# Optimization experiments

Measured on AMD Instinct MI355X. Metric: run time of the kernel, lower is better.

Reference implementation:

```python
import jax, jax.numpy as jnp
import numpy as np

LEVELS = (1, 2, 4)
NHEAD = 4
LN_EPS = 1e-5


def _layernorm(x, g, b):
    m = jnp.mean(x, axis=-1, keepdims=True)
    v = jnp.mean((x - m) ** 2, axis=-1, keepdims=True)
    return (x - m) * jax.lax.rsqrt(v + LN_EPS) * g + b


def _spp_pool(x, starts, ends):
    # Exact AdaptiveAvgPool1d over per-proposal segments via inclusive-prefix-sum.
    # x: [B,C,T]; starts/ends: [B,P] int. Returns [B, P, C*sum(LEVELS)].
    B, C, T = x.shape
    P = starts.shape[1]
    xt = jnp.transpose(x, (0, 2, 1))  # [B,T,C]
    csum = jnp.concatenate([jnp.zeros((B, 1, C), x.dtype), jnp.cumsum(xt, axis=1)], axis=1)  # [B,T+1,C]
    n = ends - starts  # [B,P], always >= 1
    feats = []
    for L in LEVELS:
        i = jnp.arange(L)
        lo = (starts[..., None] + (i * n[..., None]) // L).reshape(B, P * L)
        hi = (starts[..., None] + ((i + 1) * n[..., None] + L - 1) // L).reshape(B, P * L)
        slo = jnp.take_along_axis(csum, lo[..., None], axis=1)  # [B,P*L,C]
        shi = jnp.take_along_axis(csum, hi[..., None], axis=1)
        mean = (shi - slo) / (hi - lo).astype(x.dtype)[..., None]
        # torch view(N, C*L) flattens [C,L] C-major -> transpose bins to last axis
        feats.append(mean.reshape(B, P, L, C).transpose(0, 1, 3, 2).reshape(B, P, C * L))
    return jnp.concatenate(feats, axis=-1)


def _encoder_layer(x, qkv_w, qkv_b, out_w, out_b, g1, b1, w1, bb1, w2, bb2, g2, b2):
    # Post-norm nn.TransformerEncoderLayer with exact-erf gelu, dropout=0 (eval)
    B, P, d = x.shape
    dh = d // NHEAD
    qkv = x @ qkv_w.T + qkv_b  # [B,P,3d]
    q, k, v = jnp.split(qkv, 3, axis=-1)
    sh = lambda t: t.reshape(B, P, NHEAD, dh).transpose(0, 2, 1, 3)  # [B,H,P,dh]
    q, k, v = sh(q), sh(k), sh(v)
    scale = 1.0 / float(np.sqrt(dh))
    attn = jax.nn.softmax(jnp.einsum('bhqd,bhkd->bhqk', q, k) * scale, axis=-1)
    o = jnp.einsum('bhqk,bhkd->bhqd', attn, v).transpose(0, 2, 1, 3).reshape(B, P, d)
    o = o @ out_w.T + out_b
    x = _layernorm(x + o, g1, b1)
    h = jax.nn.gelu(x @ w1.T + bb1, approximate=False) @ w2.T + bb2
    return _layernorm(x + h, g2, b2)


def _forward(x, proposal_boxes, proj_w, proj_b, pos_w1, pos_b1, pos_w2, pos_b2,
             qkv_w, qkv_b, out_w, out_b, ln1_g, ln1_b, ff1_w, ff1_b,
             ff2_w, ff2_b, ln2_g, ln2_b, cls_w, cls_b, det_w, det_b):
    B, C, T = x.shape
    P = proposal_boxes.shape[1]
    starts = jnp.clip(proposal_boxes[..., 0], 0, T - 1)
    ends = jnp.clip(proposal_boxes[..., 1], 1, T)
    ends = jnp.where(ends <= starts, jnp.minimum(starts + 1, T), ends)
    feats = _spp_pool(x, starts, ends)  # [B,P,spp_out_dim]
    s_f = proposal_boxes[..., 0].astype(x.dtype)
    e_f = proposal_boxes[..., 1].astype(x.dtype)
    centers = (s_f + e_f) / 2.0
    lengths = jnp.maximum(e_f - s_f, 1.0)
    pos_feat = jnp.stack([centers / T, lengths / T], axis=-1)  # [B,P,2]
    sort_idx = jnp.argsort(centers, axis=1)
    feats_s = jnp.take_along_axis(feats, sort_idx[..., None], axis=1)
    pos_emb = jax.nn.relu(pos_feat @ pos_w1.T + pos_b1) @ pos_w2.T + pos_b2
    pos_emb_s = jnp.take_along_axis(pos_emb, sort_idx[..., None], axis=1)
    tok = feats_s @ proj_w.T + proj_b + pos_emb_s  # [B,P,d]
    for l in range(qkv_w.shape[0]):
        tok = _encoder_layer(tok, qkv_w[l], qkv_b[l], out_w[l], out_b[l],
                             ln1_g[l], ln1_b[l], ff1_w[l], ff1_b[l],
                             ff2_w[l], ff2_b[l], ln2_g[l], ln2_b[l])
    inv = jnp.argsort(sort_idx, axis=1)
    ctx = jnp.take_along_axis(tok, inv[..., None], axis=1)  # [B,P,d]
    class_logits = ctx @ cls_w.T + cls_b  # [B,P,nc]
    det_logits = ctx @ det_w.T + det_b
    class_prob = jax.nn.softmax(class_logits, axis=2)
    det_prob = jax.nn.softmax(det_logits, axis=1)
    joint_prob = class_prob * det_prob
    video_prob = joint_prob.sum(axis=1)
    return video_prob, joint_prob, class_logits, det_logits, ctx


def setup_inputs() -> dict:
    key = jax.random.key(0)
    ks = jax.random.split(key, 32)
    B, C, T, P = 8, 512, 2048, 512
    d, dff, nc, nl = 512, 1024, 30, 2
    spp_out = C * sum(LEVELS)
    s = 0.02
    f32 = jnp.float32
    inp = {
        'x': jax.random.normal(ks[0], (B, C, T), f32),
        'proposal_boxes': jax.random.randint(ks[1], (B, P, 2), 0, T).astype(jnp.int32),
        'proj_w': jax.random.normal(ks[2], (d, spp_out), f32) * s,
        'proj_b': jnp.zeros((d,), f32),
        'pos_w1': jax.random.normal(ks[3], (d, 2), f32) * s,
        'pos_b1': jnp.zeros((d,), f32),
        'pos_w2': jax.random.normal(ks[4], (d, d), f32) * s,
        'pos_b2': jnp.zeros((d,), f32),
        'qkv_w': jax.random.normal(ks[5], (nl, 3 * d, d), f32) * s,
        'qkv_b': jnp.zeros((nl, 3 * d), f32),
        'out_w': jax.random.normal(ks[6], (nl, d, d), f32) * s,
        'out_b': jnp.zeros((nl, d), f32),
        'ln1_g': jnp.ones((nl, d), f32),
        'ln1_b': jnp.zeros((nl, d), f32),
        'ff1_w': jax.random.normal(ks[7], (nl, dff, d), f32) * s,
        'ff1_b': jnp.zeros((nl, dff), f32),
        'ff2_w': jax.random.normal(ks[8], (nl, d, dff), f32) * s,
        'ff2_b': jnp.zeros((nl, d), f32),
        'ln2_g': jnp.ones((nl, d), f32),
        'ln2_b': jnp.zeros((nl, d), f32),
        'cls_w': jax.random.normal(ks[9], (nc, d), f32) * s,
        'cls_b': jnp.zeros((nc,), f32),
        'det_w': jax.random.normal(ks[10], (nc, d), f32) * s,
        'det_b': jnp.zeros((nc,), f32),
    }
    return inp


def reference(x, proposal_boxes, proj_w, proj_b, pos_w1, pos_b1, pos_w2, pos_b2,
              qkv_w, qkv_b, out_w, out_b, ln1_g, ln1_b, ff1_w, ff1_b,
              ff2_w, ff2_b, ln2_g, ln2_b, cls_w, cls_b, det_w, det_b):
    return _forward(x, proposal_boxes, proj_w, proj_b, pos_w1, pos_b1, pos_w2, pos_b2,
                    qkv_w, qkv_b, out_w, out_b, ln1_g, ln1_b, ff1_w, ff1_b,
                    ff2_w, ff2_b, ln2_g, ln2_b, cls_w, cls_b, det_w, det_b)
```

## Files before the change

kernel.cpp:

```cpp
#include <hip/hip_runtime.h>

#define TDIM 2048
#define CDIM 512
#define BDIM 8
#define PDIM 512
#define DMODEL 512
#define NCOUT 30
#define SPPOUT 3584
#define AKDIM 4096

typedef __attribute__((ext_vector_type(8))) short short8;
typedef __attribute__((ext_vector_type(4))) short short4v;
typedef __attribute__((ext_vector_type(4))) float f32x4;

typedef const __attribute__((address_space(1))) void* as1cv;
typedef __attribute__((address_space(3))) void* as3v;

__device__ __forceinline__ void gl_lds16(const short* g, short* l){
  __builtin_amdgcn_global_load_lds((as1cv)g, (as3v)l, 16, 0, 0);
}

__device__ __forceinline__ short f2b(float f){
  unsigned u = __float_as_uint(f);
  unsigned r = (u + 0x7fffu + ((u >> 16) & 1u)) >> 16;
  return (short)r;
}

__device__ __forceinline__ float waveSum(float v){
#pragma unroll
  for (int o = 32; o > 0; o >>= 1) v += __shfl_xor(v, o);
  return v;
}
__device__ __forceinline__ float waveMax(float v){
#pragma unroll
  for (int o = 32; o > 0; o >>= 1) v = fmaxf(v, __shfl_xor(v, o));
  return v;
}

__global__ void kprep2(const float* __restrict__ pw, const float* __restrict__ pw2,
                       const float* __restrict__ qw, const float* __restrict__ ow,
                       const float* __restrict__ f1, const float* __restrict__ f2,
                       const float* __restrict__ cl, const float* __restrict__ dt,
                       const float* __restrict__ pb, const float* __restrict__ pb2,
                       const float* __restrict__ cb, const float* __restrict__ db,
                       short* __restrict__ Wc, short* __restrict__ Wd,
                       float* __restrict__ bc, float* __restrict__ bh){
  int i = blockIdx.x * 256 + threadIdx.x;
  if (i < 2097152){
    int r = i >> 12, k = i & 4095;
    float v = (k < SPPOUT) ? pw[(size_t)r * SPPOUT + k] : pw2[(size_t)r * DMODEL + (k - SPPOUT)];
    Wc[i] = f2b(v);
  } else if (i < 6322176){
    int j = i - 2097152;
    float v;
    if (j < 1572864) v = qw[j];
    else if (j < 2097152) v = ow[j - 1572864];
    else if (j < 3145728) v = f1[j - 2097152];
    else if (j < 4194304) v = f2[j - 3145728];
    else if (j < 4209664) v = cl[j - 4194304];
    else v = dt[j - 4209664];
    Wd[j] = f2b(v);
  } else {
    int k = i - 6322176;
    if (k < 512) bc[k] = pb[k] + pb2[k];
    else if (k < 572) bh[k - 512] = (k < 542) ? cb[k - 512] : db[k - 542];
  }
}

__global__ void kscan(const float* __restrict__ x, float* __restrict__ W, float* __restrict__ tot){
  int idx = blockIdx.x;
  int b = idx >> 5, rem = idx & 31, ch = rem >> 1, cg = rem & 1;
  int c = cg * 256 + threadIdx.x;
  const float* xp = x + ((size_t)(b * CDIM + c)) * TDIM + ch * 128;
  float* wp = W + ((size_t)b * TDIM + ch * 128) * CDIM + c;
  float run = 0.f;
  for (int tl = 0; tl < 128; tl += 4){
    float4 v = *(const float4*)(xp + tl);
    run += v.x; wp[(size_t)(tl + 0) * CDIM] = run;
    run += v.y; wp[(size_t)(tl + 1) * CDIM] = run;
    run += v.z; wp[(size_t)(tl + 2) * CDIM] = run;
    run += v.w; wp[(size_t)(tl + 3) * CDIM] = run;
  }
  tot[((size_t)b * 16 + ch) * CDIM + c] = run;
}

__global__ void koff(const float* __restrict__ tot, float* __restrict__ off){
  int b = blockIdx.x >> 1, cg = blockIdx.x & 1;
  int c = cg * 256 + threadIdx.x;
  float run = 0.f;
  for (int ch = 0; ch < 16; ++ch){
    off[((size_t)b * 16 + ch) * CDIM + c] = run;
    run += tot[((size_t)b * 16 + ch) * CDIM + c];
  }
}

__global__ void ksort(const int* __restrict__ boxes, int* __restrict__ sidx, float* __restrict__ out){
  __shared__ unsigned key[PDIM];
  int b = blockIdx.x, t = threadIdx.x;
  if (b == 0 && t < 240) out[t] = 0.f;
  int s = boxes[(size_t)(b * PDIM + t) * 2];
  int e = boxes[(size_t)(b * PDIM + t) * 2 + 1];
  key[t] = ((unsigned)(s + e) << 9) | (unsigned)t;
  __syncthreads();
  for (int k = 2; k <= PDIM; k <<= 1){
    for (int j = k >> 1; j > 0; j >>= 1){
      int ixj = t ^ j;
      if (ixj > t){
        unsigned a = key[t], c2 = key[ixj];
        bool up = ((t & k) == 0);
        bool doswap = up ? (a > c2) : (a < c2);
        if (doswap){ key[t] = c2; key[ixj] = a; }
      }
      __syncthreads();
    }
  }
  sidx[b * PDIM + t] = (int)(key[t] & 511u);
}

__global__ void kspp(const float* __restrict__ W, const float* __restrict__ off,
                     const int* __restrict__ boxes, const int* __restrict__ sidx,
                     const float* __restrict__ pw1, const float* __restrict__ pb1,
                     short* __restrict__ A){
  int blk = blockIdx.x;
  int b = blk >> 9, j = blk & 511;
  int p = sidx[b * PDIM + j];
  int s0 = boxes[(size_t)(b * PDIM + p) * 2];
  int e0 = boxes[(size_t)(b * PDIM + p) * 2 + 1];
  int start = min(max(s0, 0), TDIM - 1);
  int end   = min(max(e0, 1), TDIM);
  if (end <= start) end = min(start + 1, TDIM);
  int n = end - start;

  int lo[7], hi[7], cb[7], cl[7];
  {
    const int Ls[3] = {1, 2, 4};
    const int Bo[3] = {0, 512, 1536};
    int q = 0;
    for (int li = 0; li < 3; ++li){
      int L = Ls[li];
      for (int i = 0; i < L; ++i){
        lo[q] = start + (i * n) / L;
        hi[q] = start + ((i + 1) * n + L - 1) / L;
        cb[q] = Bo[li] + i;
        cl[q] = L;
        ++q;
      }
    }
  }
  float s_f = (float)s0, e_f = (float)e0;
  float px = (s_f + e_f) * 0.5f / (float)TDIM;
  float py = fmaxf(e_f - s_f, 1.f) / (float)TDIM;
  short* Ar = A + (size_t)(b * PDIM + j) * AKDIM;
  const float* Wb = W + (size_t)b * TDIM * CDIM;
  const float* ob = off + (size_t)b * 16 * CDIM;
  for (int c = threadIdx.x; c < CDIM; c += 256){
#pragma unroll
    for (int q = 0; q < 7; ++q){
      int l = lo[q], h = hi[q];
      float fl = (l == 0) ? 0.f : (Wb[(size_t)(l - 1) * CDIM + c] + ob[((l - 1) >> 7) * CDIM + c]);
      float fh = Wb[(size_t)(h - 1) * CDIM + c] + ob[((h - 1) >> 7) * CDIM + c];
      Ar[cb[q] + c * cl[q]] = f2b((fh - fl) / (float)(h - l));
    }
    float hv = pw1[c * 2] * px + pw1[c * 2 + 1] * py + pb1[c];
    Ar[SPPOUT + c] = f2b(fmaxf(hv, 0.f));
  }
}

template<int BN, int SWZ = 0>
__global__ __launch_bounds__(256) void gemm_bt(
    int M, int N, int K,
    const short* __restrict__ A, int lda, long long sAb, long long sAh,
    const short* __restrict__ B, int ldb, long long sBb, long long sBh,
    float* __restrict__ Cf, short* __restrict__ Cb, int ldc, long long sCb, long long sCh,
    int hdiv, float alpha,
    const float* __restrict__ bias, const float* __restrict__ resid, int act,
    short* __restrict__ Vtp)
{
  constexpr int JF = BN / 32;
  __shared__ short smem[128 * 64 + BN * 64];
  short* As = smem;
  short* Bs = smem + 128 * 64;
  int bx = blockIdx.x, by = blockIdx.y, bz = blockIdx.z;
  if constexpr (SWZ){
    int nx = gridDim.x, ny = gridDim.y;
    int rt = ny >> 3;
    int flat = (bz * ny + by) * nx + bx;
    int xcd = flat & 7, wl = flat >> 3;
    by = xcd * rt + wl % rt;
    int rest = wl / rt;
    bx = rest % nx;
    bz = rest / nx;
  }
  int zb = bz / hdiv, zh = bz - zb * hdiv;
  A += (size_t)zb * sAb + (size_t)zh * sAh;
  B += (size_t)zb * sBb + (size_t)zh * sBh;
  size_t coff = (size_t)zb * sCb + (size_t)zh * sCh;
  int rowBase = by * 128, colBase = bx * BN;
  int t = threadIdx.x;
  int lane = t & 63;
  int wave = t >> 6;
  int wm = (wave >> 1) * 64, wn = (wave & 1) * (BN / 2);
  int lm = lane & 15, quad = lane >> 4;
  int srow = t >> 3;
  int skw = ((t & 7) * 8) ^ ((srow & 7) * 8);

  const short* Agp[4];
#pragma unroll
  for (int it = 0; it < 4; ++it)
    Agp[it] = A + (size_t)min(rowBase + srow + it * 32, M - 1) * lda + skw;
  const short* Bgp[JF];
#pragma unroll
  for (int it = 0; it < JF; ++it)
    Bgp[it] = B + (size_t)min(colBase + srow + it * 32, N - 1) * ldb + skw;

  f32x4 zero4 = {0.f, 0.f, 0.f, 0.f};
  f32x4 acc[4][JF];
#pragma unroll
  for (int i = 0; i < 4; ++i)
#pragma unroll
    for (int j = 0; j < JF; ++j) acc[i][j] = zero4;

  int axr = (lm & 7) * 8;
  for (int k0 = 0; k0 < K; k0 += 64){
#pragma unroll
    for (int it = 0; it < 4; ++it) gl_lds16(Agp[it] + k0, As + it * 2048 + t * 8);
#pragma unroll
    for (int it = 0; it < JF; ++it) gl_lds16(Bgp[it] + k0, Bs + it * 2048 + t * 8);
    __syncthreads();
#pragma unroll
    for (int h = 0; h < 2; ++h){
      int koff = (h * 32 + quad * 8) ^ axr;
      short8 af[4], bfr[JF];
#pragma unroll
      for (int i = 0; i < 4; ++i)
        af[i] = *(const short8*)(As + (wm + i * 16 + lm) * 64 + koff);
#pragma unroll
      for (int j = 0; j < JF; ++j)
        bfr[j] = *(const short8*)(Bs + (wn + j * 16 + lm) * 64 + koff);
#pragma unroll
      for (int i = 0; i < 4; ++i)
#pragma unroll
        for (int j = 0; j < JF; ++j)
          acc[i][j] = __builtin_amdgcn_mfma_f32_16x16x32_bf16(af[i], bfr[j], acc[i][j], 0, 0, 0);
    }
    __syncthreads();
  }

  if (Vtp && colBase >= 1024){
    short* LT = smem;
#pragma unroll
    for (int i = 0; i < 4; ++i){
#pragma unroll
      for (int j = 0; j < JF; ++j){
        int d = wn + j * 16 + lm;
        int prow = wm + i * 16 + quad * 4;
        short4v pk;
#pragma unroll
        for (int r = 0; r < 4; ++r){
          float v = acc[i][j][r] * alpha;
          if (bias) v += bias[colBase + d];
          pk[r] = f2b(v);
        }
        *(short4v*)(LT + d * 132 + prow) = pk;
      }
    }
    __syncthreads();
    int bb = rowBase >> 9;
    int hh = (colBase - 1024) >> 7;
    int dd0 = (colBase - 1024) & 127;
    int dl = t >> 2, pl = (t & 3) * 32;
    const short* sp = LT + dl * 132 + pl;
    short* dp = Vtp + ((size_t)(bb * 4 + hh)) * 65536 + (size_t)(dd0 + dl) * 512 + (rowBase & 511) + pl;
#pragma unroll
    for (int u = 0; u < 4; ++u) *(short8*)(dp + u * 8) = *(const short8*)(sp + u * 8);
    return;
  }

#pragma unroll
  for (int i = 0; i < 4; ++i){
#pragma unroll
    for (int j = 0; j < JF; ++j){
#pragma unroll
      for (int r = 0; r < 4; ++r){
        int row = rowBase + wm + i * 16 + quad * 4 + r;
        int col = colBase + wn + j * 16 + lm;
        if (row < M && col < N){
          float v = acc[i][j][r] * alpha;
          if (bias) v += bias[col];
          size_t ci = coff + (size_t)row * ldc + col;
          if (resid) v += resid[ci];
          if (act) v = 0.5f * v * (1.f + erff(v * 0.7071067811865476f));
          if (Cf) Cf[ci] = v;
          if (Cb) Cb[ci] = f2b(v);
        }
      }
    }
  }
}

__global__ void kredG1(const float* __restrict__ part, const float* __restrict__ bias,
                       float* __restrict__ tok, short* __restrict__ tokb){
  int i = blockIdx.x * 256 + threadIdx.x;
  float v = part[i] + part[i + 2097152] + part[i + 4194304] + part[i + 6291456] + bias[i & 511];
  tok[i] = v;
  tokb[i] = f2b(v);
}

__global__ __launch_bounds__(256) void kflash(const short* __restrict__ qkvb,
                                              const short* __restrict__ Vt,
                                              short* __restrict__ ob){
  __shared__ float Ofs[4][16][128];
  __shared__ float Ml[4][16], Ll[4][16], Fw[4][16], Linv[16];
  int bid = blockIdx.x;
  int bh = bid & 31, qt = bid >> 5;
  int b = bh >> 2, h = bh & 3;
  int t = threadIdx.x;
  int w = t >> 6, lane = t & 63;
  int lm = lane & 15, quad = lane >> 4;
  const float SL2 = 0.1275174468f;

  const short* qbase = qkvb + (size_t)(b * 512 + qt * 16 + lm) * 1536 + h * 128 + quad * 8;
  short8 qf[4];
#pragma unroll
  for (int s = 0; s < 4; ++s) qf[s] = *(const short8*)(qbase + s * 32);

  const short* kbase = qkvb + (size_t)(b * 512) * 1536 + 512 + h * 128 + quad * 8;
  const short* vbase = Vt + (size_t)bh * 65536 + (size_t)lm * 512 + quad * 8;

  f32x4 zero4 = {0.f, 0.f, 0.f, 0.f};
  f32x4 Of[8];
#pragma unroll
  for (int i = 0; i < 8; ++i) Of[i] = zero4;
  float mrun[4] = {-1e30f, -1e30f, -1e30f, -1e30f};
  float lrun[4] = {0.f, 0.f, 0.f, 0.f};
  short* Pw = (short*)&Ofs[w][0][0];

#pragma unroll
  for (int kt = 0; kt < 2; ++kt){
    int kb = w * 128 + kt * 64;
    f32x4 Sf[4];
#pragma unroll
    for (int j = 0; j < 4; ++j) Sf[j] = zero4;
#pragma unroll
    for (int s = 0; s < 4; ++s){
#pragma unroll
      for (int j = 0; j < 4; ++j){
        short8 kf = *(const short8*)(kbase + (size_t)(kb + j * 16 + lm) * 1536 + s * 32);
        Sf[j] = __builtin_amdgcn_mfma_f32_16x16x32_bf16(qf[s], kf, Sf[j], 0, 0, 0);
      }
    }
    float alpha[4];
#pragma unroll
    for (int r = 0; r < 4; ++r){
      float mx = fmaxf(fmaxf(Sf[0][r], Sf[1][r]), fmaxf(Sf[2][r], Sf[3][r])) * SL2;
#pragma unroll
      for (int o = 1; o < 16; o <<= 1) mx = fmaxf(mx, __shfl_xor(mx, o));
      float mnew = fmaxf(mrun[r], mx);
      alpha[r] = exp2f(mrun[r] - mnew);
      float psum = 0.f;
#pragma unroll
      for (int j = 0; j < 4; ++j){
        float p = exp2f(Sf[j][r] * SL2 - mnew);
        Sf[j][r] = p;
        psum += p;
      }
#pragma unroll
      for (int o = 1; o < 16; o <<= 1) psum += __shfl_xor(psum, o);
      lrun[r] = lrun[r] * alpha[r] + psum;
      mrun[r] = mnew;
    }
#pragma unroll
    for (int i = 0; i < 8; ++i)
#pragma unroll
      for (int r = 0; r < 4; ++r) Of[i][r] *= alpha[r];
#pragma unroll
    for (int j = 0; j < 4; ++j)
#pragma unroll
      for (int r = 0; r < 4; ++r){
        int q = quad * 4 + r;
        int key = j * 16 + lm;
        Pw[q * 64 + (key ^ ((q & 7) * 8))] = f2b(Sf[j][r]);
      }
#pragma unroll
    for (int ts = 0; ts < 2; ++ts){
      short8 pa = *(const short8*)(Pw + lm * 64 + (((ts * 32 + quad * 8) ^ ((lm & 7) * 8))));
#pragma unroll
      for (int jd = 0; jd < 8; ++jd){
        short8 vf = *(const short8*)(vbase + (size_t)(jd * 16) * 512 + kb + ts * 32);
        Of[jd] = __builtin_amdgcn_mfma_f32_16x16x32_bf16(pa, vf, Of[jd], 0, 0, 0);
      }
    }
  }

#pragma unroll
  for (int jd = 0; jd < 8; ++jd)
#pragma unroll
    for (int r = 0; r < 4; ++r)
      Ofs[w][quad * 4 + r][jd * 16 + lm] = Of[jd][r];
  if (lm == 0){
#pragma unroll
    for (int r = 0; r < 4; ++r){
      Ml[w][quad * 4 + r] = mrun[r];
      Ll[w][quad * 4 + r] = lrun[r];
    }
  }
  __syncthreads();

  if (t < 64){
    int wv = t >> 4, row = t & 15;
    float M = fmaxf(fmaxf(Ml[0][row], Ml[1][row]), fmaxf(Ml[2][row], Ml[3][row]));
    Fw[wv][row] = exp2f(Ml[wv][row] - M);
    if (wv == 0){
      float lsum = Ll[0][row] * exp2f(Ml[0][row] - M) + Ll[1][row] * exp2f(Ml[1][row] - M)
                 + Ll[2][row] * exp2f(Ml[2][row] - M) + Ll[3][row] * exp2f(Ml[3][row] - M);
      Linv[row] = 1.f / lsum;
    }
  }
  __syncthreads();

  {
    int row = t >> 4, dbase = (t & 15) * 8;
    float f0 = Fw[0][row], f1 = Fw[1][row], f2v = Fw[2][row], f3 = Fw[3][row];
    float li = Linv[row];
    short* dst = ob + ((size_t)(b * 512 + qt * 16 + row)) * 512 + h * 128 + dbase;
#pragma unroll
    for (int u = 0; u < 8; ++u){
      float v = Ofs[0][row][dbase + u] * f0 + Ofs[1][row][dbase + u] * f1
              + Ofs[2][row][dbase + u] * f2v + Ofs[3][row][dbase + u] * f3;
      dst[u] = f2b(v * li);
    }
  }
}

__global__ void klnR(const float* __restrict__ part, const float* __restrict__ bias,
                     const float* __restrict__ resid,
                     const float* __restrict__ g, const float* __restrict__ bb,
                     float* __restrict__ Yf, short* __restrict__ Yb){
  int row = blockIdx.x, lane = threadIdx.x;
  size_t base = (size_t)row * DMODEL;
  float v[8]; float s = 0.f;
#pragma unroll
  for (int i = 0; i < 8; ++i){
    int c = lane + 64 * i;
    v[i] = part[base + c] + part[base + c + 2097152] + part[base + c + 4194304]
         + part[base + c + 6291456] + bias[c] + resid[base + c];
    s += v[i];
  }
  s = waveSum(s);
  float m = s * (1.f / DMODEL);
  float q = 0.f;
#pragma unroll
  for (int i = 0; i < 8; ++i){ float d = v[i] - m; q += d * d; }
  q = waveSum(q);
  float inv = rsqrtf(q * (1.f / DMODEL) + 1e-5f);
#pragma unroll
  for (int i = 0; i < 8; ++i){
    int c = lane + 64 * i;
    float o = (v[i] - m) * inv * g[c] + bb[c];
    Yf[base + c] = o;
    Yb[base + c] = f2b(o);
  }
}

__global__ void kdetsm(const float* __restrict__ hd, float* __restrict__ dp){
  int b = blockIdx.x / NCOUT, c = blockIdx.x % NCOUT, lane = threadIdx.x;
  float v[8]; float m = -1e30f;
#pragma unroll
  for (int i = 0; i < 8; ++i){
    v[i] = hd[((size_t)(b * PDIM) + lane + 64 * i) * 60 + 30 + c];
    m = fmaxf(m, v[i]);
  }
  m = waveMax(m);
  float s = 0.f;
#pragma unroll
  for (int i = 0; i < 8; ++i){ v[i] = expf(v[i] - m); s += v[i]; }
  s = waveSum(s);
  float r = 1.f / s;
#pragma unroll
  for (int i = 0; i < 8; ++i)
    dp[((size_t)(b * PDIM) + lane + 64 * i) * NCOUT + c] = v[i] * r;
}

__global__ void kfinal(const float* __restrict__ hd, const float* __restrict__ dps,
                       const float* __restrict__ tok, const int* __restrict__ sidx,
                       float* __restrict__ out){
  int blk = blockIdx.x;
  int b = blk >> 9, j = blk & 511;
  int lane = threadIdx.x;
  int p = sidx[b * PDIM + j];
  float* video = out;
  float* joint = out + 240;
  float* clso  = out + 123120;
  float* deto  = out + 246000;
  float* ctxo  = out + 368880;
  size_t rs60 = (size_t)(b * PDIM + j) * 60;
  size_t rs30 = (size_t)(b * PDIM + j) * NCOUT;
  size_t ro = (size_t)(b * PDIM + p) * NCOUT;
  float lc = (lane < NCOUT) ? hd[rs60 + lane] : -1e30f;
  float m = waveMax(lc);
  float e = (lane < NCOUT) ? expf(lc - m) : 0.f;
  float s = waveSum(e);
  float cp = e / s;
  if (lane < NCOUT){
    float dv  = hd[rs60 + 30 + lane];
    float dpv = dps[rs30 + lane];
    float jp  = cp * dpv;
    clso[ro + lane] = lc;
    deto[ro + lane] = dv;
    joint[ro + lane] = jp;
    atomicAdd(&video[b * NCOUT + lane], jp);
  }
  const float* tr = tok + (size_t)(b * PDIM + j) * DMODEL;
  float* cr = ctxo + (size_t)(b * PDIM + p) * DMODEL;
  for (int c = lane; c < DMODEL; c += 64) cr[c] = tr[c];
}

extern "C" void kernel_launch(void* const* d_in, const int* in_sizes, int n_in,
                              void* d_out, int out_size, void* d_ws, size_t ws_size,
                              hipStream_t stream) {
  const float* x      = (const float*)d_in[0];
  const int*   boxes  = (const int*)d_in[1];
  const float* proj_w = (const float*)d_in[2];
  const float* proj_b = (const float*)d_in[3];
  const float* pos_w1 = (const float*)d_in[4];
  const float* pos_b1 = (const float*)d_in[5];
  const float* pos_w2 = (const float*)d_in[6];
  const float* pos_b2 = (const float*)d_in[7];
  const float* qkv_w  = (const float*)d_in[8];
  const float* qkv_b  = (const float*)d_in[9];
  const float* out_w  = (const float*)d_in[10];
  const float* out_b  = (const float*)d_in[11];
  const float* ln1_g  = (const float*)d_in[12];
  const float* ln1_b  = (const float*)d_in[13];
  const float* ff1_w  = (const float*)d_in[14];
  const float* ff1_b  = (const float*)d_in[15];
  const float* ff2_w  = (const float*)d_in[16];
  const float* ff2_b  = (const float*)d_in[17];
  const float* ln2_g  = (const float*)d_in[18];
  const float* ln2_b  = (const float*)d_in[19];
  const float* cls_w  = (const float*)d_in[20];
  const float* cls_b  = (const float*)d_in[21];
  const float* det_w  = (const float*)d_in[22];
  const float* det_b  = (const float*)d_in[23];
  float* out = (float*)d_out;
  float* ws  = (float*)d_ws;

  const size_t oR1    = 0;
  const size_t oS     = 9437184;
  const size_t oTok   = 22020096;
  const size_t oTokb  = 24117248;
  const size_t oTok2  = 25165824;
  const size_t oTok2b = 27262976;
  const size_t oWcat  = 28311552;
  const size_t oBcat  = 29360128;
  const size_t oWq    = 29360640;
  const size_t oWo    = 30147072;
  const size_t oWf1   = 30409216;
  const size_t oWf2   = 30933504;
  const size_t oWcls  = 31457792;
  const size_t oTot   = 31473152;
  const size_t oOff   = 31538688;
  const size_t oSidx  = 31604224;
  const size_t oBhead = oTot;

  short* Abf   = (short*)(ws + oR1);
  short* qkvb  = (short*)(ws + oR1);
  short* Vt    = (short*)(ws + oR1 + 3145728);
  short* obufb = (short*)(ws + oR1 + 4194304);
  short* hbufb = (short*)(ws + oR1 + 5242880);
  float* headS = ws + oR1 + 7340032;
  float* dpS   = ws + oR1 + 7585792;
  float* csum  = ws + oS;
  float* Cpart = ws + oS;
  float* Cp2   = ws + oS;
  float* tok   = ws + oTok;
  short* tokb  = (short*)(ws + oTokb);
  float* tok2  = ws + oTok2;
  short* tok2b = (short*)(ws + oTok2b);
  short* Wcatb = (short*)(ws + oWcat);
  float* bcat  = ws + oBcat;
  short* Wq    = (short*)(ws + oWq);
  short* Wo    = (short*)(ws + oWo);
  short* Wf1   = (short*)(ws + oWf1);
  short* Wf2   = (short*)(ws + oWf2);
  short* Whead = (short*)(ws + oWcls);
  float* tot   = ws + oTot;
  float* offp  = ws + oOff;
  int*   sidx  = (int*)(ws + oSidx);
  float* bhead = ws + oBhead;

  kscan<<<256, 256, 0, stream>>>(x, csum, tot);
  koff<<<16, 256, 0, stream>>>(tot, offp);
  ksort<<<BDIM, 512, 0, stream>>>(boxes, sidx, out);
  kprep2<<<24699, 256, 0, stream>>>(proj_w, pos_w2, qkv_w, out_w, ff1_w, ff2_w, cls_w, det_w,
                                    proj_b, pos_b2, cls_b, det_b, Wcatb, Wq, bcat, bhead);
  kspp<<<BDIM * PDIM, 256, 0, stream>>>(csum, offp, boxes, sidx, pos_w1, pos_b1, Abf);

  gemm_bt<64, 1><<<dim3(8, 32, 4), 256, 0, stream>>>(
      4096, 512, 1024, Abf, 4096, 1024, 0, Wcatb, 4096, 1024, 0,
      Cpart, nullptr, 512, 2097152, 0, 1, 1.f, nullptr, nullptr, 0, nullptr);
  kredG1<<<8192, 256, 0, stream>>>(Cpart, bcat, tok, tokb);

  for (int l = 0; l < 2; ++l){
    const short* qw  = Wq  + (size_t)l * 1536 * 512;
    const short* ow  = Wo  + (size_t)l * 512 * 512;
    const short* f1w = Wf1 + (size_t)l * 1024 * 512;
    const short* f2w = Wf2 + (size_t)l * 512 * 1024;
    const float* qb  = qkv_b + (size_t)l * 1536;
    const float* obv = out_b + (size_t)l * 512;
    const float* f1b = ff1_b + (size_t)l * 1024;
    const float* f2b_ = ff2_b + (size_t)l * 512;

    gemm_bt<64><<<dim3(24, 32, 1), 256, 0, stream>>>(
        4096, 1536, 512, tokb, 512, 0, 0, qw, 512, 0, 0,
        nullptr, qkvb, 1536, 0, 0, 1, 1.f, qb, nullptr, 0, Vt);
    kflash<<<1024, 256, 0, stream>>>(qkvb, Vt, obufb);
    gemm_bt<64><<<dim3(8, 32, 4), 256, 0, stream>>>(
        4096, 512, 128, obufb, 512, 128, 0, ow, 512, 128, 0,
        Cp2, nullptr, 512, 2097152, 0, 1, 1.f, nullptr, nullptr, 0, nullptr);
    klnR<<<4096, 64, 0, stream>>>(Cp2, obv, tok, ln1_g + l * 512, ln1_b + l * 512, tok2, tok2b);
    gemm_bt<64><<<dim3(16, 32, 1), 256, 0, stream>>>(
        4096, 1024, 512, tok2b, 512, 0, 0, f1w, 512, 0, 0,
        nullptr, hbufb, 1024, 0, 0, 1, 1.f, f1b, nullptr, 1, nullptr);
    gemm_bt<64><<<dim3(8, 32, 4), 256, 0, stream>>>(
        4096, 512, 256, hbufb, 1024, 256, 0, f2w, 1024, 256, 0,
        Cp2, nullptr, 512, 2097152, 0, 1, 1.f, nullptr, nullptr, 0, nullptr);
    klnR<<<4096, 64, 0, stream>>>(Cp2, f2b_, tok2, ln2_g + l * 512, ln2_b + l * 512, tok, tokb);
  }

  gemm_bt<64><<<dim3(1, 32, 1), 256, 0, stream>>>(
      4096, 60, 512, tokb, 512, 0, 0, Whead, 512, 0, 0,
      headS, nullptr, 60, 0, 0, 1, 1.f, bhead, nullptr, 0, nullptr);
  kdetsm<<<BDIM * NCOUT, 64, 0, stream>>>(headS, dpS);
  kfinal<<<BDIM * PDIM, 64, 0, stream>>>(headS, dpS, tok, sidx, out);
}
```

Measured before the change: 522.6 us.

## Fuse prep kernels, move offsets into kspp, halve split-K, vectorize reductions

```diff
diff --git a/kernel.cpp b/kernel.cpp
--- a/kernel.cpp
+++ b/kernel.cpp
@@ -37,92 +37,97 @@
   return v;
 }
 
-__global__ void kprep2(const float* __restrict__ pw, const float* __restrict__ pw2,
-                       const float* __restrict__ qw, const float* __restrict__ ow,
-                       const float* __restrict__ f1, const float* __restrict__ f2,
-                       const float* __restrict__ cl, const float* __restrict__ dt,
-                       const float* __restrict__ pb, const float* __restrict__ pb2,
-                       const float* __restrict__ cb, const float* __restrict__ db,
-                       short* __restrict__ Wc, short* __restrict__ Wd,
-                       float* __restrict__ bc, float* __restrict__ bh){
-  int i = blockIdx.x * 256 + threadIdx.x;
-  if (i < 2097152){
-    int r = i >> 12, k = i & 4095;
-    float v = (k < SPPOUT) ? pw[(size_t)r * SPPOUT + k] : pw2[(size_t)r * DMODEL + (k - SPPOUT)];
-    Wc[i] = f2b(v);
-  } else if (i < 6322176){
-    int j = i - 2097152;
-    float v;
-    if (j < 1572864) v = qw[j];
-    else if (j < 2097152) v = ow[j - 1572864];
-    else if (j < 3145728) v = f1[j - 2097152];
-    else if (j < 4194304) v = f2[j - 3145728];
-    else if (j < 4209664) v = cl[j - 4194304];
-    else v = dt[j - 4209664];
-    Wd[j] = f2b(v);
+__global__ __launch_bounds__(512) void k0(
+    const float* __restrict__ x, const int* __restrict__ boxes,
+    const float* __restrict__ pw, const float* __restrict__ pw2,
+    const float* __restrict__ qw, const float* __restrict__ ow,
+    const float* __restrict__ f1, const float* __restrict__ f2,
+    const float* __restrict__ cl, const float* __restrict__ dt,
+    const float* __restrict__ pb, const float* __restrict__ pb2,
+    const float* __restrict__ cb, const float* __restrict__ db,
+    float* __restrict__ W, float* __restrict__ tot,
+    int* __restrict__ sidx, float* __restrict__ out,
+    short* __restrict__ Wc, short* __restrict__ Wd,
+    float* __restrict__ bc, float* __restrict__ bh)
+{
+  __shared__ unsigned key[PDIM];
+  int blk = blockIdx.x, t = threadIdx.x;
+  if (blk < 128){
+    int b = blk >> 4, ch = blk & 15;
+    int c = t;
+    const float* xp = x + ((size_t)(b * CDIM + c)) * TDIM + ch * 128;
+    float* wp = W + ((size_t)b * TDIM + ch * 128) * CDIM + c;
+    float run = 0.f;
+    for (int tl = 0; tl < 128; tl += 4){
+      float4 v = *(const float4*)(xp + tl);
+      run += v.x; wp[(size_t)(tl + 0) * CDIM] = run;
+      run += v.y; wp[(size_t)(tl + 1) * CDIM] = run;
+      run += v.z; wp[(size_t)(tl + 2) * CDIM] = run;
+      run += v.w; wp[(size_t)(tl + 3) * CDIM] = run;
+    }
+    tot[((size_t)b * 16 + ch) * CDIM + c] = run;
+  } else if (blk < 136){
+    int b = blk - 128;
+    if (b == 0 && t < 240) out[t] = 0.f;
+    int s = boxes[(size_t)(b * PDIM + t) * 2];
+    int e = boxes[(size_t)(b * PDIM + t) * 2 + 1];
+    key[t] = ((unsigned)(s + e) << 9) | (unsigned)t;
+    __syncthreads();
+    for (int k = 2; k <= PDIM; k <<= 1){
+      for (int j = k >> 1; j > 0; j >>= 1){
+        int ixj = t ^ j;
+        if (ixj > t){
+          unsigned a = key[t], c2 = key[ixj];
+          bool up = ((t & k) == 0);
+          bool doswap = up ? (a > c2) : (a < c2);
+          if (doswap){ key[t] = c2; key[ixj] = a; }
+        }
+        __syncthreads();
+      }
+    }
+    sidx[b * PDIM + t] = (int)(key[t] & 511u);
   } else {
-    int k = i - 6322176;
-    if (k < 512) bc[k] = pb[k] + pb2[k];
-    else if (k < 572) bh[k - 512] = (k < 542) ? cb[k - 512] : db[k - 542];
-  }
-}
-
-__global__ void kscan(const float* __restrict__ x, float* __restrict__ W, float* __restrict__ tot){
-  int idx = blockIdx.x;
-  int b = idx >> 5, rem = idx & 31, ch = rem >> 1, cg = rem & 1;
-  int c = cg * 256 + threadIdx.x;
-  const float* xp = x + ((size_t)(b * CDIM + c)) * TDIM + ch * 128;
-  float* wp = W + ((size_t)b * TDIM + ch * 128) * CDIM + c;
-  float run = 0.f;
-  for (int tl = 0; tl < 128; tl += 4){
-    float4 v = *(const float4*)(xp + tl);
-    run += v.x; wp[(size_t)(tl + 0) * CDIM] = run;
-    run += v.y; wp[(size_t)(tl + 1) * CDIM] = run;
-    run += v.z; wp[(size_t)(tl + 2) * CDIM] = run;
-    run += v.w; wp[(size_t)(tl + 3) * CDIM] = run;
-  }
-  tot[((size_t)b * 16 + ch) * CDIM + c] = run;
-}
-
-__global__ void koff(const float* __restrict__ tot, float* __restrict__ off){
-  int b = blockIdx.x >> 1, cg = blockIdx.x & 1;
-  int c = cg * 256 + threadIdx.x;
-  float run = 0.f;
-  for (int ch = 0; ch < 16; ++ch){
-    off[((size_t)b * 16 + ch) * CDIM + c] = run;
-    run += tot[((size_t)b * 16 + ch) * CDIM + c];
-  }
-}
-
-__global__ void ksort(const int* __restrict__ boxes, int* __restrict__ sidx, float* __restrict__ out){
-  __shared__ unsigned key[PDIM];
-  int b = blockIdx.x, t = threadIdx.x;
-  if (b == 0 && t < 240) out[t] = 0.f;
-  int s = boxes[(size_t)(b * PDIM + t) * 2];
-  int e = boxes[(size_t)(b * PDIM + t) * 2 + 1];
-  key[t] = ((unsigned)(s + e) << 9) | (unsigned)t;
-  __syncthreads();
-  for (int k = 2; k <= PDIM; k <<= 1){
-    for (int j = k >> 1; j > 0; j >>= 1){
-      int ixj = t ^ j;
-      if (ixj > t){
-        unsigned a = key[t], c2 = key[ixj];
-        bool up = ((t & k) == 0);
-        bool doswap = up ? (a > c2) : (a < c2);
-        if (doswap){ key[t] = c2; key[ixj] = a; }
-      }
-      __syncthreads();
-    }
-  }
-  sidx[b * PDIM + t] = (int)(key[t] & 511u);
-}
-
-__global__ void kspp(const float* __restrict__ W, const float* __restrict__ off,
+    int i = (blk - 136) * 512 + t;
+    if (i < 2097152){
+      int r = i >> 12, k = i & 4095;
+      float v = (k < SPPOUT) ? pw[(size_t)r * SPPOUT + k] : pw2[(size_t)r * DMODEL + (k - SPPOUT)];
+      Wc[i] = f2b(v);
+    } else if (i < 6322176){
+      int j = i - 2097152;
+      float v;
+      if (j < 1572864) v = qw[j];
+      else if (j < 2097152) v = ow[j - 1572864];
+      else if (j < 3145728) v = f1[j - 2097152];
+      else if (j < 4194304) v = f2[j - 3145728];
+      else if (j < 4209664) v = cl[j - 4194304];
+      else v = dt[j - 4209664];
+      Wd[j] = f2b(v);
+    } else {
+      int k = i - 6322176;
+      if (k < 512) bc[k] = pb[k] + pb2[k];
+      else if (k < 572) bh[k - 512] = (k < 542) ? cb[k - 512] : db[k - 542];
+    }
+  }
+}
+
+__global__ void kspp(const float* __restrict__ W, const float* __restrict__ tot,
                      const int* __restrict__ boxes, const int* __restrict__ sidx,
                      const float* __restrict__ pw1, const float* __restrict__ pb1,
                      short* __restrict__ A){
+  __shared__ float offs[16][CDIM];
   int blk = blockIdx.x;
   int b = blk >> 9, j = blk & 511;
+#pragma unroll
+  for (int half = 0; half < 2; ++half){
+    int cc = threadIdx.x + half * 256;
+    float run = 0.f;
+#pragma unroll
+    for (int ch = 0; ch < 16; ++ch){
+      offs[ch][cc] = run;
+      run += tot[((size_t)b * 16 + ch) * CDIM + cc];
+    }
+  }
+  __syncthreads();
   int p = sidx[b * PDIM + j];
   int s0 = boxes[(size_t)(b * PDIM + p) * 2];
   int e0 = boxes[(size_t)(b * PDIM + p) * 2 + 1];
@@ -152,13 +157,12 @@
   float py = fmaxf(e_f - s_f, 1.f) / (float)TDIM;
   short* Ar = A + (size_t)(b * PDIM + j) * AKDIM;
   const float* Wb = W + (size_t)b * TDIM * CDIM;
-  const float* ob = off + (size_t)b * 16 * CDIM;
   for (int c = threadIdx.x; c < CDIM; c += 256){
 #pragma unroll
     for (int q = 0; q < 7; ++q){
       int l = lo[q], h = hi[q];
-      float fl = (l == 0) ? 0.f : (Wb[(size_t)(l - 1) * CDIM + c] + ob[((l - 1) >> 7) * CDIM + c]);
-      float fh = Wb[(size_t)(h - 1) * CDIM + c] + ob[((h - 1) >> 7) * CDIM + c];
+      float fl = (l == 0) ? 0.f : (Wb[(size_t)(l - 1) * CDIM + c] + offs[(l - 1) >> 7][c]);
+      float fh = Wb[(size_t)(h - 1) * CDIM + c] + offs[(h - 1) >> 7][c];
       Ar[cb[q] + c * cl[q]] = f2b((fh - fl) / (float)(h - l));
     }
     float hv = pw1[c * 2] * px + pw1[c * 2 + 1] * py + pb1[c];
@@ -300,10 +304,18 @@
 
 __global__ void kredG1(const float* __restrict__ part, const float* __restrict__ bias,
                        float* __restrict__ tok, short* __restrict__ tokb){
-  int i = blockIdx.x * 256 + threadIdx.x;
-  float v = part[i] + part[i + 2097152] + part[i + 4194304] + part[i + 6291456] + bias[i & 511];
-  tok[i] = v;
-  tokb[i] = f2b(v);
+  int idx = blockIdx.x * 256 + threadIdx.x;
+  const float4* p = (const float4*)part;
+  float4 v0 = p[idx], v1 = p[idx + 524288], v2 = p[idx + 1048576], v3 = p[idx + 1572864];
+  float4 bv = ((const float4*)bias)[idx & 127];
+  float4 v;
+  v.x = v0.x + v1.x + v2.x + v3.x + bv.x;
+  v.y = v0.y + v1.y + v2.y + v3.y + bv.y;
+  v.z = v0.z + v1.z + v2.z + v3.z + bv.z;
+  v.w = v0.w + v1.w + v2.w + v3.w + bv.w;
+  ((float4*)tok)[idx] = v;
+  short4v s4 = { f2b(v.x), f2b(v.y), f2b(v.z), f2b(v.w) };
+  *(short4v*)(tokb + (size_t)idx * 4) = s4;
 }
 
 __global__ __launch_bounds__(256) void kflash(const short* __restrict__ qkvb,
@@ -442,8 +454,7 @@
 #pragma unroll
   for (int i = 0; i < 8; ++i){
     int c = lane + 64 * i;
-    v[i] = part[base + c] + part[base + c + 2097152] + part[base + c + 4194304]
-         + part[base + c + 6291456] + bias[c] + resid[base + c];
+    v[i] = part[base + c] + part[base + c + 2097152] + bias[c] + resid[base + c];
     s += v[i];
   }
   s = waveSum(s);
@@ -473,12 +484,12 @@
   m = waveMax(m);
   float s = 0.f;
 #pragma unroll
-  for (int i = 0; i < 8; ++i){ v[i] = expf(v[i] - m); s += v[i]; }
+  for (int i = 0; i < 8; ++i){ s += expf(v[i] - m); }
   s = waveSum(s);
-  float r = 1.f / s;
-#pragma unroll
-  for (int i = 0; i < 8; ++i)
-    dp[((size_t)(b * PDIM) + lane + 64 * i) * NCOUT + c] = v[i] * r;
+  if (lane == 0){
+    dp[b * NCOUT + c] = m;
+    dp[240 + b * NCOUT + c] = 1.f / s;
+  }
 }
 
 __global__ void kfinal(const float* __restrict__ hd, const float* __restrict__ dps,
@@ -494,7 +505,6 @@
   float* deto  = out + 246000;
   float* ctxo  = out + 368880;
   size_t rs60 = (size_t)(b * PDIM + j) * 60;
-  size_t rs30 = (size_t)(b * PDIM + j) * NCOUT;
   size_t ro = (size_t)(b * PDIM + p) * NCOUT;
   float lc = (lane < NCOUT) ? hd[rs60 + lane] : -1e30f;
   float m = waveMax(lc);
@@ -503,16 +513,16 @@
   float cp = e / s;
   if (lane < NCOUT){
     float dv  = hd[rs60 + 30 + lane];
-    float dpv = dps[rs30 + lane];
+    float dpv = expf(dv - dps[b * NCOUT + lane]) * dps[240 + b * NCOUT + lane];
     float jp  = cp * dpv;
     clso[ro + lane] = lc;
     deto[ro + lane] = dv;
     joint[ro + lane] = jp;
     atomicAdd(&video[b * NCOUT + lane], jp);
   }
-  const float* tr = tok + (size_t)(b * PDIM + j) * DMODEL;
-  float* cr = ctxo + (size_t)(b * PDIM + p) * DMODEL;
-  for (int c = lane; c < DMODEL; c += 64) cr[c] = tr[c];
+  const float4* tr = (const float4*)(tok + (size_t)(b * PDIM + j) * DMODEL);
+  float4* cr = (float4*)(ctxo + (size_t)(b * PDIM + p) * DMODEL);
+  for (int c = lane; c < DMODEL / 4; c += 64) cr[c] = tr[c];
 }
 
 extern "C" void kernel_launch(void* const* d_in, const int* in_sizes, int n_in,
@@ -559,9 +569,8 @@
   const size_t oWf2   = 30933504;
   const size_t oWcls  = 31457792;
   const size_t oTot   = 31473152;
-  const size_t oOff   = 31538688;
   const size_t oSidx  = 31604224;
-  const size_t oBhead = oTot;
+  const size_t oBhead = oTot + 65536;
 
   short* Abf   = (short*)(ws + oR1);
   short* qkvb  = (short*)(ws + oR1);
@@ -585,21 +594,18 @@
   short* Wf2   = (short*)(ws + oWf2);
   short* Whead = (short*)(ws + oWcls);
   float* tot   = ws + oTot;
-  float* offp  = ws + oOff;
   int*   sidx  = (int*)(ws + oSidx);
   float* bhead = ws + oBhead;
 
-  kscan<<<256, 256, 0, stream>>>(x, csum, tot);
-  koff<<<16, 256, 0, stream>>>(tot, offp);
-  ksort<<<BDIM, 512, 0, stream>>>(boxes, sidx, out);
-  kprep2<<<24699, 256, 0, stream>>>(proj_w, pos_w2, qkv_w, out_w, ff1_w, ff2_w, cls_w, det_w,
-                                    proj_b, pos_b2, cls_b, det_b, Wcatb, Wq, bcat, bhead);
-  kspp<<<BDIM * PDIM, 256, 0, stream>>>(csum, offp, boxes, sidx, pos_w1, pos_b1, Abf);
+  k0<<<12486, 512, 0, stream>>>(x, boxes, proj_w, pos_w2, qkv_w, out_w, ff1_w, ff2_w,
+                                cls_w, det_w, proj_b, pos_b2, cls_b, det_b,
+                                csum, tot, sidx, out, Wcatb, Wq, bcat, bhead);
+  kspp<<<BDIM * PDIM, 256, 0, stream>>>(csum, tot, boxes, sidx, pos_w1, pos_b1, Abf);
 
   gemm_bt<64, 1><<<dim3(8, 32, 4), 256, 0, stream>>>(
       4096, 512, 1024, Abf, 4096, 1024, 0, Wcatb, 4096, 1024, 0,
       Cpart, nullptr, 512, 2097152, 0, 1, 1.f, nullptr, nullptr, 0, nullptr);
-  kredG1<<<8192, 256, 0, stream>>>(Cpart, bcat, tok, tokb);
+  kredG1<<<2048, 256, 0, stream>>>(Cpart, bcat, tok, tokb);
 
   for (int l = 0; l < 2; ++l){
     const short* qw  = Wq  + (size_t)l * 1536 * 512;
@@ -615,15 +621,15 @@
         4096, 1536, 512, tokb, 512, 0, 0, qw, 512, 0, 0,
         nullptr, qkvb, 1536, 0, 0, 1, 1.f, qb, nullptr, 0, Vt);
     kflash<<<1024, 256, 0, stream>>>(qkvb, Vt, obufb);
-    gemm_bt<64><<<dim3(8, 32, 4), 256, 0, stream>>>(
-        4096, 512, 128, obufb, 512, 128, 0, ow, 512, 128, 0,
+    gemm_bt<64><<<dim3(8, 32, 2), 256, 0, stream>>>(
+        4096, 512, 256, obufb, 512, 256, 0, ow, 512, 256, 0,
         Cp2, nullptr, 512, 2097152, 0, 1, 1.f, nullptr, nullptr, 0, nullptr);
     klnR<<<4096, 64, 0, stream>>>(Cp2, obv, tok, ln1_g + l * 512, ln1_b + l * 512, tok2, tok2b);
     gemm_bt<64><<<dim3(16, 32, 1), 256, 0, stream>>>(
         4096, 1024, 512, tok2b, 512, 0, 0, f1w, 512, 0, 0,
         nullptr, hbufb, 1024, 0, 0, 1, 1.f, f1b, nullptr, 1, nullptr);
-    gemm_bt<64><<<dim3(8, 32, 4), 256, 0, stream>>>(
-        4096, 512, 256, hbufb, 1024, 256, 0, f2w, 1024, 256, 0,
+    gemm_bt<64><<<dim3(8, 32, 2), 256, 0, stream>>>(
+        4096, 512, 512, hbufb, 1024, 512, 0, f2w, 1024, 512, 0,
         Cp2, nullptr, 512, 2097152, 0, 1, 1.f, nullptr, nullptr, 0, nullptr);
     klnR<<<4096, 64, 0, stream>>>(Cp2, f2b_, tok2, ln2_g + l * 512, ln2_b + l * 512, tok, tokb);
   }
```

Result: faster. 506.9 us (-3.0%).
